# Performance work log

Hardware: AMD Instinct MI355X
Metric: run time of the kernel (lower is better)

## Reference

```python
import jax, jax.numpy as jnp
import numpy as np

B = 256      # batch size
V = 50257    # vocab size (rows of indices index into [0, V))


def setup_inputs() -> dict:
    key = jax.random.key(0)
    k1, k2 = jax.random.split(key)
    indices = jax.random.randint(k1, (B, V), 0, V)                 # [B, V] int
    w_es = jax.random.normal(k2, (B, V), dtype=jnp.float32)        # [B, V] float
    return {"indices": indices, "w_es": w_es}


def reference(indices, w_es):
    # weighting_scheme = row-wise softmax: weights [B, V]
    weights = jax.nn.softmax(w_es, axis=-1)
    Bb, Vv = indices.shape
    # average[b, indices[b, i]] += weights[b, i]  -- weighted one-hot scatter-accumulate,
    # replacing the original Python loop over voc_size with a single batched scatter-add.
    average = jnp.zeros((Bb, Vv), dtype=w_es.dtype).at[
        jnp.arange(Bb)[:, None], indices
    ].add(weights)
    # original returns the transposed weights [V, B]
    return (average, weights.T)
```

## Files before the change

kernel.cpp:

```cpp
#include <hip/hip_runtime.h>
#include <math.h>

#define BB 256
#define VV 50257

__global__ __launch_bounds__(1024) void row_stats_kernel(
    const float* __restrict__ w, float2* __restrict__ stats, int V)
{
    const int b = blockIdx.x;
    const float* row = w + (size_t)b * V;
    const int tid = threadIdx.x; const int nt = 1024;

    const int a = (int)(((16u - ((uintptr_t)row & 15u)) & 15u) >> 2);
    const int nv4 = (V - a) >> 2;
    const float4* rv = (const float4*)(row + a);
    const int tail0 = a + (nv4 << 2);

    float m0 = -INFINITY, m1 = -INFINITY, m2 = -INFINITY, m3 = -INFINITY;
    for (int i = tid; i < a; i += nt) m0 = fmaxf(m0, row[i]);
    for (int i = tail0 + tid; i < V; i += nt) m0 = fmaxf(m0, row[i]);
    {
        int i = tid;
        for (; i + 3 * nt < nv4; i += 4 * nt) {
            float4 v0 = rv[i], v1 = rv[i + nt], v2 = rv[i + 2 * nt], v3 = rv[i + 3 * nt];
            m0 = fmaxf(m0, fmaxf(fmaxf(v0.x, v0.y), fmaxf(v0.z, v0.w)));
            m1 = fmaxf(m1, fmaxf(fmaxf(v1.x, v1.y), fmaxf(v1.z, v1.w)));
            m2 = fmaxf(m2, fmaxf(fmaxf(v2.x, v2.y), fmaxf(v2.z, v2.w)));
            m3 = fmaxf(m3, fmaxf(fmaxf(v3.x, v3.y), fmaxf(v3.z, v3.w)));
        }
        for (; i < nv4; i += nt) {
            float4 v0 = rv[i];
            m0 = fmaxf(m0, fmaxf(fmaxf(v0.x, v0.y), fmaxf(v0.z, v0.w)));
        }
    }
    float m = fmaxf(fmaxf(m0, m1), fmaxf(m2, m3));
    #pragma unroll
    for (int off = 32; off >= 1; off >>= 1) m = fmaxf(m, __shfl_xor(m, off, 64));
    __shared__ float sred[16];
    __shared__ float ssum[16];
    const int wave = tid >> 6, lane = tid & 63;
    if (lane == 0) sred[wave] = m;
    __syncthreads();
    float M = sred[0];
    #pragma unroll
    for (int i = 1; i < 16; ++i) M = fmaxf(M, sred[i]);

    float s0 = 0.f, s1 = 0.f, s2 = 0.f, s3 = 0.f;
    for (int i = tid; i < a; i += nt) s0 += __expf(row[i] - M);
    for (int i = tail0 + tid; i < V; i += nt) s0 += __expf(row[i] - M);
    {
        int i = tid;
        for (; i + 3 * nt < nv4; i += 4 * nt) {
            float4 v0 = rv[i], v1 = rv[i + nt], v2 = rv[i + 2 * nt], v3 = rv[i + 3 * nt];
            s0 += __expf(v0.x - M) + __expf(v0.y - M) + __expf(v0.z - M) + __expf(v0.w - M);
            s1 += __expf(v1.x - M) + __expf(v1.y - M) + __expf(v1.z - M) + __expf(v1.w - M);
            s2 += __expf(v2.x - M) + __expf(v2.y - M) + __expf(v2.z - M) + __expf(v2.w - M);
            s3 += __expf(v3.x - M) + __expf(v3.y - M) + __expf(v3.z - M) + __expf(v3.w - M);
        }
        for (; i < nv4; i += nt) {
            float4 v0 = rv[i];
            s0 += __expf(v0.x - M) + __expf(v0.y - M) + __expf(v0.z - M) + __expf(v0.w - M);
        }
    }
    float s = (s0 + s1) + (s2 + s3);
    #pragma unroll
    for (int off = 32; off >= 1; off >>= 1) s += __shfl_xor(s, off, 64);
    if (lane == 0) ssum[wave] = s;
    __syncthreads();
    if (tid == 0) {
        float S = 0.f;
        #pragma unroll
        for (int i = 0; i < 16; ++i) S += ssum[i];
        stats[b] = make_float2(M, 1.0f / S);
    }
}

#define NRANGE 4
#define QSZ 12565

__global__ __launch_bounds__(512) void scatter_kernel(
    const float* __restrict__ w, const int* __restrict__ idx,
    const float2* __restrict__ stats, float* __restrict__ avg, int V)
{
    __shared__ float acc[QSZ];

    const int bid  = blockIdx.x;
    const int xcd  = bid & 7;
    const int slot = bid >> 3;
    const int row  = xcd + 8 * (slot >> 2);
    const int q    = slot & 3;
    const int lo   = q * QSZ;
    const int hi   = min(V, lo + QSZ);
    const unsigned range = (unsigned)(hi - lo);
    const int tid  = threadIdx.x; const int nt = 512;

    for (int i = tid; i < QSZ; i += nt) acc[i] = 0.f;
    const float2 st = stats[row];
    const float M = st.x, inv = st.y;
    __syncthreads();

    const size_t base = (size_t)row * V;
    const float* wr = w + base;
    const int*   ir = idx + base;
    const int a = (int)(((16u - ((uintptr_t)wr & 15u)) & 15u) >> 2);
    const int nv4 = (V - a) >> 2;
    const int tail0 = a + (nv4 << 2);
    const float4* wv4 = (const float4*)(wr + a);
    const int4*   iv4 = (const int4*)(ir + a);

#define PROC1(idv, xv)                                                     \
    do {                                                                   \
        unsigned off = (unsigned)((idv) - lo);                             \
        if (off < range) atomicAdd(&acc[off], __expf((xv) - M) * inv);     \
    } while (0)
#define PROC4(iv, xv)                                                      \
    do {                                                                   \
        PROC1((iv).x, (xv).x); PROC1((iv).y, (xv).y);                      \
        PROC1((iv).z, (xv).z); PROC1((iv).w, (xv).w);                      \
    } while (0)

    for (int i = tid; i < a; i += nt) PROC1(ir[i], wr[i]);
    for (int i = tail0 + tid; i < V; i += nt) PROC1(ir[i], wr[i]);

    {
        int i = tid;
        for (; i + 3 * nt < nv4; i += 4 * nt) {
            int4   i0 = iv4[i], i1 = iv4[i + nt], i2 = iv4[i + 2 * nt], i3 = iv4[i + 3 * nt];
            float4 x0 = wv4[i], x1 = wv4[i + nt], x2 = wv4[i + 2 * nt], x3 = wv4[i + 3 * nt];
            PROC4(i0, x0); PROC4(i1, x1); PROC4(i2, x2); PROC4(i3, x3);
        }
        for (; i < nv4; i += nt) {
            int4 i0 = iv4[i]; float4 x0 = wv4[i];
            PROC4(i0, x0);
        }
    }
    __syncthreads();

    for (int i = tid; i < hi - lo; i += nt)
        __builtin_nontemporal_store(acc[i], &avg[base + lo + i]);
#undef PROC1
#undef PROC4
}

#define T3V 64
#define T3B 64

__global__ __launch_bounds__(256) void transpose_kernel(
    const float* __restrict__ w, const float2* __restrict__ stats,
    float* __restrict__ wT, int Bn, int V)
{
    __shared__ float tile[T3V][T3B + 1];
    __shared__ float sM[T3B], sI[T3B];

    const int v0 = blockIdx.x * T3V;
    const int b0 = blockIdx.y * T3B;
    const int tid = threadIdx.x;

    if (tid < T3B) { float2 st = stats[b0 + tid]; sM[tid] = st.x; sI[tid] = st.y; }
    __syncthreads();

    const int tx = tid & 63;
    const int ty = tid >> 6;
    const int v  = v0 + tx;
    const bool vok = (v < V);

    #pragma unroll
    for (int it = 0; it < T3B / 4; ++it) {
        const int bl = ty + 4 * it;
        float wgt = 0.f;
        if (vok) {
            const float x = w[(size_t)(b0 + bl) * V + v];
            wgt = __expf(x - sM[bl]) * sI[bl];
        }
        tile[tx][bl] = wgt;
    }
    __syncthreads();

    const int bx = tid & 63;
    const int vy = tid >> 6;
    #pragma unroll
    for (int it = 0; it < T3V / 4; ++it) {
        const int vr = vy + 4 * it;
        const int v2 = v0 + vr;
        if (v2 < V) __builtin_nontemporal_store(tile[vr][bx], &wT[(size_t)v2 * Bn + b0 + bx]);
    }
}

extern "C" void kernel_launch(void* const* d_in, const int* in_sizes, int n_in,
                              void* d_out, int out_size, void* d_ws, size_t ws_size,
                              hipStream_t stream) {
    const int*   indices = (const int*)d_in[0];
    const float* w_es    = (const float*)d_in[1];
    float* avg = (float*)d_out;
    float* wT  = (float*)d_out + (size_t)BB * VV;
    float2* stats = (float2*)d_ws;

    row_stats_kernel<<<BB, 1024, 0, stream>>>(w_es, stats, VV);

    scatter_kernel<<<BB * NRANGE, 512, 0, stream>>>(w_es, indices, stats, avg, VV);

    dim3 g3((VV + T3V - 1) / T3V, BB / T3B);
    transpose_kernel<<<g3, 256, 0, stream>>>(w_es, stats, wT, BB, VV);
}
```

Measured before the change: 250.0 us.

## Split row stats across blocks, fold softmax into exp2 offset, widen scatter ranges

The row-stats pass now runs four blocks per row, each producing a partial max and sum, and a small combine kernel merges them into one log-normaliser per row. The scatter and transpose kernels compute weights as exp2(x*log2e - C), so no separate multiply by the inverse sum is needed. The scatter kernel now uses two 25K-entry LDS ranges per row with 1024 threads instead of four ranges. Out-of-range hits are sent to per-lane dummy slots rather than guarded by a branch, and the main loop is unrolled to eight. These changes aim for more parallelism in the stats pass and half as many redundant index/weight reads in the scatter. The costs are an extra kernel launch, larger LDS use per block, and atomic work on dummy slots.

```diff
diff --git a/kernel.cpp b/kernel.cpp
--- a/kernel.cpp
+++ b/kernel.cpp
@@ -3,63 +3,74 @@
 
 #define BB 256
 #define VV 50257
-
-__global__ __launch_bounds__(1024) void row_stats_kernel(
-    const float* __restrict__ w, float2* __restrict__ stats, int V)
-{
-    const int b = blockIdx.x;
-    const float* row = w + (size_t)b * V;
-    const int tid = threadIdx.x; const int nt = 1024;
-
-    const int a = (int)(((16u - ((uintptr_t)row & 15u)) & 15u) >> 2);
-    const int nv4 = (V - a) >> 2;
-    const float4* rv = (const float4*)(row + a);
+#define L2E 1.4426950408889634f
+
+#define QS 12576
+
+__global__ __launch_bounds__(512) void partial_stats_kernel(
+    const float* __restrict__ w, float2* __restrict__ partial, int V)
+{
+    const int bid = blockIdx.x;
+    const int row = bid >> 2, q = bid & 3;
+    const int lo = q * QS, hi = min(V, lo + QS);
+    const int n = hi - lo;
+    const float* p = w + (size_t)row * V + lo;
+    const int tid = threadIdx.x; const int nt = 512;
+
+    const int a = (int)(((16u - ((uintptr_t)p & 15u)) & 15u) >> 2);
+    const int nv4 = (n - a) >> 2;
+    const float4* pv = (const float4*)(p + a);
     const int tail0 = a + (nv4 << 2);
 
     float m0 = -INFINITY, m1 = -INFINITY, m2 = -INFINITY, m3 = -INFINITY;
-    for (int i = tid; i < a; i += nt) m0 = fmaxf(m0, row[i]);
-    for (int i = tail0 + tid; i < V; i += nt) m0 = fmaxf(m0, row[i]);
+    for (int i = tid; i < a; i += nt) m0 = fmaxf(m0, p[i]);
+    for (int i = tail0 + tid; i < n; i += nt) m0 = fmaxf(m0, p[i]);
     {
         int i = tid;
         for (; i + 3 * nt < nv4; i += 4 * nt) {
-            float4 v0 = rv[i], v1 = rv[i + nt], v2 = rv[i + 2 * nt], v3 = rv[i + 3 * nt];
+            float4 v0 = pv[i], v1 = pv[i + nt], v2 = pv[i + 2 * nt], v3 = pv[i + 3 * nt];
             m0 = fmaxf(m0, fmaxf(fmaxf(v0.x, v0.y), fmaxf(v0.z, v0.w)));
             m1 = fmaxf(m1, fmaxf(fmaxf(v1.x, v1.y), fmaxf(v1.z, v1.w)));
             m2 = fmaxf(m2, fmaxf(fmaxf(v2.x, v2.y), fmaxf(v2.z, v2.w)));
             m3 = fmaxf(m3, fmaxf(fmaxf(v3.x, v3.y), fmaxf(v3.z, v3.w)));
         }
         for (; i < nv4; i += nt) {
-            float4 v0 = rv[i];
+            float4 v0 = pv[i];
             m0 = fmaxf(m0, fmaxf(fmaxf(v0.x, v0.y), fmaxf(v0.z, v0.w)));
         }
     }
     float m = fmaxf(fmaxf(m0, m1), fmaxf(m2, m3));
     #pragma unroll
     for (int off = 32; off >= 1; off >>= 1) m = fmaxf(m, __shfl_xor(m, off, 64));
-    __shared__ float sred[16];
-    __shared__ float ssum[16];
+    __shared__ float sred[8], ssum[8];
     const int wave = tid >> 6, lane = tid & 63;
     if (lane == 0) sred[wave] = m;
     __syncthreads();
     float M = sred[0];
     #pragma unroll
-    for (int i = 1; i < 16; ++i) M = fmaxf(M, sred[i]);
+    for (int i = 1; i < 8; ++i) M = fmaxf(M, sred[i]);
+    const float mML2 = -M * L2E;
 
     float s0 = 0.f, s1 = 0.f, s2 = 0.f, s3 = 0.f;
-    for (int i = tid; i < a; i += nt) s0 += __expf(row[i] - M);
-    for (int i = tail0 + tid; i < V; i += nt) s0 += __expf(row[i] - M);
+    for (int i = tid; i < a; i += nt) s0 += exp2f(fmaf(p[i], L2E, mML2));
+    for (int i = tail0 + tid; i < n; i += nt) s0 += exp2f(fmaf(p[i], L2E, mML2));
     {
         int i = tid;
         for (; i + 3 * nt < nv4; i += 4 * nt) {
-            float4 v0 = rv[i], v1 = rv[i + nt], v2 = rv[i + 2 * nt], v3 = rv[i + 3 * nt];
-            s0 += __expf(v0.x - M) + __expf(v0.y - M) + __expf(v0.z - M) + __expf(v0.w - M);
-            s1 += __expf(v1.x - M) + __expf(v1.y - M) + __expf(v1.z - M) + __expf(v1.w - M);
-            s2 += __expf(v2.x - M) + __expf(v2.y - M) + __expf(v2.z - M) + __expf(v2.w - M);
-            s3 += __expf(v3.x - M) + __expf(v3.y - M) + __expf(v3.z - M) + __expf(v3.w - M);
+            float4 v0 = pv[i], v1 = pv[i + nt], v2 = pv[i + 2 * nt], v3 = pv[i + 3 * nt];
+            s0 += exp2f(fmaf(v0.x, L2E, mML2)) + exp2f(fmaf(v0.y, L2E, mML2))
+                + exp2f(fmaf(v0.z, L2E, mML2)) + exp2f(fmaf(v0.w, L2E, mML2));
+            s1 += exp2f(fmaf(v1.x, L2E, mML2)) + exp2f(fmaf(v1.y, L2E, mML2))
+                + exp2f(fmaf(v1.z, L2E, mML2)) + exp2f(fmaf(v1.w, L2E, mML2));
+            s2 += exp2f(fmaf(v2.x, L2E, mML2)) + exp2f(fmaf(v2.y, L2E, mML2))
+                + exp2f(fmaf(v2.z, L2E, mML2)) + exp2f(fmaf(v2.w, L2E, mML2));
+            s3 += exp2f(fmaf(v3.x, L2E, mML2)) + exp2f(fmaf(v3.y, L2E, mML2))
+                + exp2f(fmaf(v3.z, L2E, mML2)) + exp2f(fmaf(v3.w, L2E, mML2));
         }
         for (; i < nv4; i += nt) {
-            float4 v0 = rv[i];
-            s0 += __expf(v0.x - M) + __expf(v0.y - M) + __expf(v0.z - M) + __expf(v0.w - M);
+            float4 v0 = pv[i];
+            s0 += exp2f(fmaf(v0.x, L2E, mML2)) + exp2f(fmaf(v0.y, L2E, mML2))
+                + exp2f(fmaf(v0.z, L2E, mML2)) + exp2f(fmaf(v0.w, L2E, mML2));
         }
     }
     float s = (s0 + s1) + (s2 + s3);
@@ -70,33 +81,43 @@
     if (tid == 0) {
         float S = 0.f;
         #pragma unroll
-        for (int i = 0; i < 16; ++i) S += ssum[i];
-        stats[b] = make_float2(M, 1.0f / S);
-    }
-}
-
-#define NRANGE 4
-#define QSZ 12565
-
-__global__ __launch_bounds__(512) void scatter_kernel(
+        for (int i = 0; i < 8; ++i) S += ssum[i];
+        partial[bid] = make_float2(M, S);
+    }
+}
+
+__global__ void combine_kernel(const float2* __restrict__ partial, float* __restrict__ Cc)
+{
+    const int b = threadIdx.x;
+    float2 p0 = partial[b * 4 + 0], p1 = partial[b * 4 + 1];
+    float2 p2 = partial[b * 4 + 2], p3 = partial[b * 4 + 3];
+    float M = fmaxf(fmaxf(p0.x, p1.x), fmaxf(p2.x, p3.x));
+    float S = p0.y * exp2f((p0.x - M) * L2E) + p1.y * exp2f((p1.x - M) * L2E)
+            + p2.y * exp2f((p2.x - M) * L2E) + p3.y * exp2f((p3.x - M) * L2E);
+    Cc[b] = M * L2E + log2f(S);
+}
+
+#define RS 25152
+
+__global__ __launch_bounds__(1024, 4) void scatter_kernel(
     const float* __restrict__ w, const int* __restrict__ idx,
-    const float2* __restrict__ stats, float* __restrict__ avg, int V)
-{
-    __shared__ float acc[QSZ];
-
-    const int bid  = blockIdx.x;
-    const int xcd  = bid & 7;
-    const int slot = bid >> 3;
-    const int row  = xcd + 8 * (slot >> 2);
-    const int q    = slot & 3;
-    const int lo   = q * QSZ;
-    const int hi   = min(V, lo + QSZ);
+    const float* __restrict__ Cc, float* __restrict__ avg, int V)
+{
+    __shared__ float acc[RS + 64];
+
+    const int bid = blockIdx.x;
+    const int xcd = bid & 7;
+    const int s   = bid >> 3;
+    const int row = xcd + 8 * (s >> 1);
+    const int q   = s & 1;
+    const int lo  = q * RS;
+    const int hi  = min(V, lo + RS);
     const unsigned range = (unsigned)(hi - lo);
-    const int tid  = threadIdx.x; const int nt = 512;
-
-    for (int i = tid; i < QSZ; i += nt) acc[i] = 0.f;
-    const float2 st = stats[row];
-    const float M = st.x, inv = st.y;
+    const int tid = threadIdx.x; const int nt = 1024;
+
+    for (int i = tid; i < RS; i += nt) acc[i] = 0.f;
+    const float mC = -Cc[row];
+    const unsigned dummy = (unsigned)(RS + (tid & 63));
     __syncthreads();
 
     const size_t base = (size_t)row * V;
@@ -108,36 +129,43 @@
     const float4* wv4 = (const float4*)(wr + a);
     const int4*   iv4 = (const int4*)(ir + a);
 
-#define PROC1(idv, xv)                                                     \
-    do {                                                                   \
-        unsigned off = (unsigned)((idv) - lo);                             \
-        if (off < range) atomicAdd(&acc[off], __expf((xv) - M) * inv);     \
+#define PROC1(idv, xv)                                                          \
+    do {                                                                        \
+        unsigned off = (unsigned)(idv) - (unsigned)lo;                          \
+        unsigned slot = (off < range) ? off : dummy;    \
+        atomicAdd(&acc[slot], exp2f(fmaf((xv), L2E, mC)));                      \
     } while (0)
-#define PROC4(iv, xv)                                                      \
-    do {                                                                   \
-        PROC1((iv).x, (xv).x); PROC1((iv).y, (xv).y);                      \
-        PROC1((iv).z, (xv).z); PROC1((iv).w, (xv).w);                      \
+#define PROC4(iv, xv)                                                           \
+    do {                                                                        \
+        PROC1((iv).x, (xv).x); PROC1((iv).y, (xv).y);                           \
+        PROC1((iv).z, (xv).z); PROC1((iv).w, (xv).w);                           \
     } while (0)
 
     for (int i = tid; i < a; i += nt) PROC1(ir[i], wr[i]);
     for (int i = tail0 + tid; i < V; i += nt) PROC1(ir[i], wr[i]);
 
-    {
-        int i = tid;
-        for (; i + 3 * nt < nv4; i += 4 * nt) {
-            int4   i0 = iv4[i], i1 = iv4[i + nt], i2 = iv4[i + 2 * nt], i3 = iv4[i + 3 * nt];
-            float4 x0 = wv4[i], x1 = wv4[i + nt], x2 = wv4[i + 2 * nt], x3 = wv4[i + 3 * nt];
-            PROC4(i0, x0); PROC4(i1, x1); PROC4(i2, x2); PROC4(i3, x3);
-        }
-        for (; i < nv4; i += nt) {
-            int4 i0 = iv4[i]; float4 x0 = wv4[i];
-            PROC4(i0, x0);
-        }
-    }
-    __syncthreads();
-
-    for (int i = tid; i < hi - lo; i += nt)
-        __builtin_nontemporal_store(acc[i], &avg[base + lo + i]);
+    int i = tid;
+    for (; i + 7 * nt < nv4; i += 8 * nt) {
+        int4   i0 = iv4[i],          i1 = iv4[i + nt],     i2 = iv4[i + 2 * nt], i3 = iv4[i + 3 * nt];
+        int4   i4 = iv4[i + 4 * nt], i5 = iv4[i + 5 * nt], i6 = iv4[i + 6 * nt], i7 = iv4[i + 7 * nt];
+        float4 x0 = wv4[i],          x1 = wv4[i + nt],     x2 = wv4[i + 2 * nt], x3 = wv4[i + 3 * nt];
+        float4 x4 = wv4[i + 4 * nt], x5 = wv4[i + 5 * nt], x6 = wv4[i + 6 * nt], x7 = wv4[i + 7 * nt];
+        PROC4(i0, x0); PROC4(i1, x1); PROC4(i2, x2); PROC4(i3, x3);
+        PROC4(i4, x4); PROC4(i5, x5); PROC4(i6, x6); PROC4(i7, x7);
+    }
+    for (; i + 3 * nt < nv4; i += 4 * nt) {
+        int4   i0 = iv4[i], i1 = iv4[i + nt], i2 = iv4[i + 2 * nt], i3 = iv4[i + 3 * nt];
+        float4 x0 = wv4[i], x1 = wv4[i + nt], x2 = wv4[i + 2 * nt], x3 = wv4[i + 3 * nt];
+        PROC4(i0, x0); PROC4(i1, x1); PROC4(i2, x2); PROC4(i3, x3);
+    }
+    for (; i < nv4; i += nt) {
+        int4 i0 = iv4[i]; float4 x0 = wv4[i];
+        PROC4(i0, x0);
+    }
+    __syncthreads();
+
+    for (int j = tid; j < (int)range; j += nt)
+        __builtin_nontemporal_store(acc[j], &avg[base + lo + j]);
 #undef PROC1
 #undef PROC4
 }
@@ -146,17 +174,17 @@
 #define T3B 64
 
 __global__ __launch_bounds__(256) void transpose_kernel(
-    const float* __restrict__ w, const float2* __restrict__ stats,
+    const float* __restrict__ w, const float* __restrict__ Cc,
     float* __restrict__ wT, int Bn, int V)
 {
     __shared__ float tile[T3V][T3B + 1];
-    __shared__ float sM[T3B], sI[T3B];
+    __shared__ float sC[T3B];
 
     const int v0 = blockIdx.x * T3V;
     const int b0 = blockIdx.y * T3B;
     const int tid = threadIdx.x;
 
-    if (tid < T3B) { float2 st = stats[b0 + tid]; sM[tid] = st.x; sI[tid] = st.y; }
+    if (tid < T3B) sC[tid] = -Cc[b0 + tid];
     __syncthreads();
 
     const int tx = tid & 63;
@@ -170,7 +198,7 @@
         float wgt = 0.f;
         if (vok) {
             const float x = w[(size_t)(b0 + bl) * V + v];
-            wgt = __expf(x - sM[bl]) * sI[bl];
+            wgt = exp2f(fmaf(x, L2E, sC[bl]));
         }
         tile[tx][bl] = wgt;
     }
@@ -193,12 +221,13 @@
     const float* w_es    = (const float*)d_in[1];
     float* avg = (float*)d_out;
     float* wT  = (float*)d_out + (size_t)BB * VV;
-    float2* stats = (float2*)d_ws;
-
-    row_stats_kernel<<<BB, 1024, 0, stream>>>(w_es, stats, VV);
-
-    scatter_kernel<<<BB * NRANGE, 512, 0, stream>>>(w_es, indices, stats, avg, VV);
-
-    dim3 g3((VV + T3V - 1) / T3V, BB / T3B);
-    transpose_kernel<<<g3, 256, 0, stream>>>(w_es, stats, wT, BB, VV);
-}
+    float2* partial = (float2*)d_ws;
+    float*  Cc      = (float*)((char*)d_ws + 1024 * sizeof(float2));
+
+    partial_stats_kernel<<<BB * 4, 512, 0, stream>>>(w_es, partial, VV);
+    combine_kernel<<<1, BB, 0, stream>>>(partial, Cc);
+    scatter_kernel<<<BB * 2, 1024, 0, stream>>>(w_es, indices, Cc, avg, VV);
+
+    dim3 g4((VV + T3V - 1) / T3V, BB / T3B);
+    transpose_kernel<<<g4, 256, 0, stream>>>(w_es, Cc, wT, BB, VV);
+}
```

Result: slower. 316.3 us (+26.5%).
